# Performance work log

Measured on AMD Instinct MI355X. Metric: run time of the kernel, lower is better.

The kernel has to match this reference:

```python
import jax, jax.numpy as jnp
import numpy as np

B, C, D, H, W = 1, 32, 32, 128, 128


def setup_inputs() -> dict:
    key = jax.random.key(0)
    kx, kq, kk, kv, ko = jax.random.split(key, 5)
    s = 1.0 / np.sqrt(C)
    return {
        "x": jax.random.normal(kx, (B, C, D, H, W), dtype=jnp.float32),
        "Wq": jax.random.normal(kq, (C, C), dtype=jnp.float32) * s,
        "Wk": jax.random.normal(kk, (C, C), dtype=jnp.float32) * s,
        "Wv": jax.random.normal(kv, (C, C), dtype=jnp.float32) * s,
        "Wo": jax.random.normal(ko, (C, C), dtype=jnp.float32) * s,
    }


def reference(x, Wq, Wk, Wv, Wo):
    # x: [B, C, D, H, W]; multi-dimensional (axial) self-attention:
    # independent softmax-attention along each spatial axis, outputs summed.
    scale = jnp.asarray(x.shape[1], x.dtype) ** -0.5
    q = jnp.einsum("bcdhw,oc->bodhw", x, Wq)
    k = jnp.einsum("bcdhw,oc->bodhw", x, Wk)
    v = jnp.einsum("bcdhw,oc->bodhw", x, Wv)

    # attention along D axis: scores [B, H, W, D, D]
    ad = jax.nn.softmax(jnp.einsum("bcdhw,bcehw->bhwde", q, k) * scale, axis=-1)
    od = jnp.einsum("bhwde,bcehw->bcdhw", ad, v)

    # attention along H axis: scores [B, D, W, H, H]
    ah = jax.nn.softmax(jnp.einsum("bcdhw,bcdgw->bdwhg", q, k) * scale, axis=-1)
    oh = jnp.einsum("bdwhg,bcdgw->bcdhw", ah, v)

    # attention along W axis: scores [B, D, H, W, W]
    aw = jax.nn.softmax(jnp.einsum("bcdhw,bcdhu->bdhwu", q, k) * scale, axis=-1)
    ow = jnp.einsum("bdhwu,bcdhu->bcdhw", aw, v)

    out = jnp.einsum("bcdhw,oc->bodhw", od + oh + ow, Wo) + x  # residual
    return out
```

## Files before the change

### kernel.cpp

```cpp
#include <hip/hip_runtime.h>


#define C_ 32
#define D_ 32
#define H_ 128
#define W_ 128
#define SC (D_*H_*W_)
#define SD (H_*W_)
#define SH (W_)
#define SCALE 0.17677669529663687f

typedef __attribute__((ext_vector_type(8))) short short8;
typedef __attribute__((ext_vector_type(4))) short short4v;
typedef __attribute__((ext_vector_type(2))) short short2v;
typedef __attribute__((ext_vector_type(4))) float f32x4;

#define MFMA16(a,b,c) __builtin_amdgcn_mfma_f32_16x16x32_bf16(a,b,c,0,0,0)

__device__ __forceinline__ int xcd_swz(int bid, int nwg) {
    int chunk = nwg >> 3;
    return (bid & 7) * chunk + (bid >> 3);
}
__device__ __forceinline__ short bf16_trunc(float f) {
    return (short)(__float_as_uint(f) >> 16);
}
__device__ __forceinline__ short bf16_rtne(float f) {
    unsigned u = __float_as_uint(f);
    unsigned r = u + 0x7FFFu + ((u >> 16) & 1u);
    return (short)(r >> 16);
}
__device__ __forceinline__ float bf16_tof(short s) {
    return __uint_as_float(((unsigned)(unsigned short)s) << 16);
}
__device__ __forceinline__ short8 ld8_b64x2(const short* p) {
    short4v a = *(const short4v*)p;
    short4v b = *(const short4v*)(p + 4);
    short8 o;
    o[0]=a[0]; o[1]=a[1]; o[2]=a[2]; o[3]=a[3];
    o[4]=b[0]; o[5]=b[1]; o[6]=b[2]; o[7]=b[3];
    return o;
}

__device__ __forceinline__ void compute_Mbf(const float* __restrict__ Wq,
                                            const float* __restrict__ Wk,
                                            short* Mh, short* Ml) {
    for (int o = threadIdx.x; o < 1024; o += 256) {
        int a = o >> 5, b = o & 31;
        float acc = 0.f;
        #pragma unroll
        for (int m = 0; m < 32; ++m) acc += Wq[m*32+a] * Wk[m*32+b];
        acc *= SCALE;
        short h = bf16_trunc(acc);
        Mh[o] = h;
        Ml[o] = bf16_trunc(acc - bf16_tof(h));
    }
}
__device__ __forceinline__ void compute_Pbf(const float* __restrict__ Wv,
                                            const float* __restrict__ Wo,
                                            short* Ph, short* Pl) {
    for (int o = threadIdx.x; o < 1024; o += 256) {
        int oo = o >> 5, c = o & 31;
        float acc = 0.f;
        #pragma unroll
        for (int m = 0; m < 32; ++m) acc += Wo[oo*32+m] * Wv[m*32+c];
        short h = bf16_trunc(acc);
        Ph[o] = h;
        Pl[o] = bf16_trunc(acc - bf16_tof(h));
    }
}

#define TT_STRIDE 40
#define XH_STRIDE 136
#define P_STRIDE  136
#define R_BYTES   36864

__device__ __forceinline__ void slice_engine(
        const float* Xf, const short* Mh, const short* Ml,
        short* Tt_h, short* Tt_l, short* P, short* Xh,
        f32x4 uacc[2][2])
{
    const int t = threadIdx.x;
    const int wv = t >> 6, l = t & 63, hi = l >> 4, r = l & 15;
    const int qb = wv * 32;

    #pragma unroll
    for (int k = 0; k < 8; ++k) {
        int idx = t + k*256;
        int u2 = idx & 63, c = idx >> 6;
        float2 v = *(const float2*)&Xf[c*128 + u2*2];
        short2v h; h[0] = bf16_rtne(v.x); h[1] = bf16_rtne(v.y);
        *(short2v*)&Xh[c*XH_STRIDE + u2*2] = h;
    }

    short8 xh_[2], xl_[2];
    #pragma unroll
    for (int nt = 0; nt < 2; ++nt) {
        int u = qb + nt*16 + r;
        #pragma unroll
        for (int j = 0; j < 8; ++j) {
            float f = Xf[(hi*8 + j)*128 + u];
            short h = bf16_trunc(f);
            xh_[nt][j] = h; xl_[nt][j] = bf16_trunc(f - bf16_tof(h));
        }
    }

    short8 mah[2], mal[2];
    #pragma unroll
    for (int mt = 0; mt < 2; ++mt) {
        mah[mt] = *(const short8*)&Mh[(r + 16*mt)*32 + hi*8];
        mal[mt] = *(const short8*)&Ml[(r + 16*mt)*32 + hi*8];
    }
    f32x4 tacc[2][2] = {};
    #pragma unroll
    for (int nt = 0; nt < 2; ++nt) {
        #pragma unroll
        for (int mt = 0; mt < 2; ++mt) {
            tacc[mt][nt] = MFMA16(mah[mt], xh_[nt], tacc[mt][nt]);
            tacc[mt][nt] = MFMA16(mah[mt], xl_[nt], tacc[mt][nt]);
            tacc[mt][nt] = MFMA16(mal[mt], xh_[nt], tacc[mt][nt]);
        }
    }
    #pragma unroll
    for (int mt = 0; mt < 2; ++mt)
    #pragma unroll
    for (int nt = 0; nt < 2; ++nt) {
        int u = qb + nt*16 + r;
        #pragma unroll
        for (int rp = 0; rp < 2; ++rp) {
            int c0 = 16*mt + 4*hi + 2*rp;
            float f0 = tacc[mt][nt][2*rp], f1 = tacc[mt][nt][2*rp+1];
            short h0 = bf16_trunc(f0), h1 = bf16_trunc(f1);
            short2v vh; vh[0] = h0; vh[1] = h1;
            *(short2v*)&Tt_h[u*TT_STRIDE + c0] = vh;
            short2v vl; vl[0] = bf16_trunc(f0 - bf16_tof(h0));
            vl[1] = bf16_trunc(f1 - bf16_tof(h1));
            *(short2v*)&Tt_l[u*TT_STRIDE + c0] = vl;
        }
    }
    __syncthreads();

    f32x4 sacc[2][8] = {};
    #pragma unroll
    for (int nt = 0; nt < 8; ++nt) {
        short8 th = *(const short8*)&Tt_h[(nt*16 + r)*TT_STRIDE + hi*8];
        short8 tl = *(const short8*)&Tt_l[(nt*16 + r)*TT_STRIDE + hi*8];
        #pragma unroll
        for (int qt = 0; qt < 2; ++qt) {
            sacc[qt][nt] = MFMA16(xh_[qt], th, sacc[qt][nt]);
            sacc[qt][nt] = MFMA16(xh_[qt], tl, sacc[qt][nt]);
            sacc[qt][nt] = MFMA16(xl_[qt], th, sacc[qt][nt]);
        }
    }
    float rls[2][4];
    #pragma unroll
    for (int qt = 0; qt < 2; ++qt)
    #pragma unroll
    for (int reg = 0; reg < 4; ++reg) {
        float m = sacc[qt][0][reg];
        #pragma unroll
        for (int nt = 1; nt < 8; ++nt) m = fmaxf(m, sacc[qt][nt][reg]);
        m = fmaxf(m, __shfl_xor(m, 1));
        m = fmaxf(m, __shfl_xor(m, 2));
        m = fmaxf(m, __shfl_xor(m, 4));
        m = fmaxf(m, __shfl_xor(m, 8));
        float s = 0.f;
        #pragma unroll
        for (int nt = 0; nt < 8; ++nt) {
            float e = __expf(sacc[qt][nt][reg] - m);
            sacc[qt][nt][reg] = e; s += e;
        }
        s += __shfl_xor(s, 1);
        s += __shfl_xor(s, 2);
        s += __shfl_xor(s, 4);
        s += __shfl_xor(s, 8);
        rls[qt][reg] = 1.f / s;
    }
    __syncthreads();
    #pragma unroll
    for (int qt = 0; qt < 2; ++qt)
    #pragma unroll
    for (int reg = 0; reg < 4; ++reg) {
        int q = qb + 16*qt + 4*hi + reg;
        float rl = rls[qt][reg];
        #pragma unroll
        for (int nt = 0; nt < 8; ++nt)
            P[q*P_STRIDE + nt*16 + r] = bf16_rtne(sacc[qt][nt][reg] * rl);
    }
    __syncthreads();

    #pragma unroll
    for (int kt = 0; kt < 4; ++kt) {
        short8 xa[2], pb[2];
        #pragma unroll
        for (int mt = 0; mt < 2; ++mt)
            xa[mt] = *(const short8*)&Xh[(r + 16*mt)*XH_STRIDE + hi*8 + kt*32];
        #pragma unroll
        for (int nt = 0; nt < 2; ++nt)
            pb[nt] = *(const short8*)&P[(qb + 16*nt + r)*P_STRIDE + hi*8 + kt*32];
        #pragma unroll
        for (int mt = 0; mt < 2; ++mt)
        #pragma unroll
        for (int nt = 0; nt < 2; ++nt)
            uacc[mt][nt] = MFMA16(xa[mt], pb[nt], uacc[mt][nt]);
    }
}

__global__ __launch_bounds__(256) void kw_kernel(const float* __restrict__ x,
        const float* __restrict__ Wq, const float* __restrict__ Wk,
        float* __restrict__ U) {
    __shared__ __align__(16) char Rr[R_BYTES];
    __shared__ __align__(16) short Xh[32*XH_STRIDE];
    __shared__ __align__(16) short MhS[1024], MlS[1024];
    float* Xf = (float*)Rr;
    short* Tt_h = (short*)(Rr + 16384);
    short* Tt_l = (short*)(Rr + 26624);
    short* P = (short*)Rr;
    int bid = xcd_swz(blockIdx.x, gridDim.x);
    int d = bid >> 7, h = bid & 127;
    int t = threadIdx.x;
    compute_Mbf(Wq, Wk, MhS, MlS);
    const float* xs = x + d*SD + h*SH;
    #pragma unroll
    for (int k = 0; k < 4; ++k) {
        int idx = t + k*256;
        int c = idx >> 5, u4 = idx & 31;
        *(float4*)&Xf[c*128 + u4*4] = *(const float4*)&xs[c*SC + u4*4];
    }
    __syncthreads();
    f32x4 uacc[2][2] = {};
    slice_engine(Xf, MhS, MlS, Tt_h, Tt_l, P, Xh, uacc);
    const int wv = t >> 6, l = t & 63, hi = l >> 4, r = l & 15;
    float* Uo = U + d*SD + h*SH;
    #pragma unroll
    for (int mt = 0; mt < 2; ++mt)
    #pragma unroll
    for (int nt = 0; nt < 2; ++nt)
    #pragma unroll
    for (int reg = 0; reg < 4; ++reg) {
        int c = 16*mt + 4*hi + reg;
        int q = wv*32 + 16*nt + r;
        Uo[c*SC + q] = uacc[mt][nt][reg];
    }
}

__global__ __launch_bounds__(256) void kh_kernel(const float* __restrict__ x,
        const float* __restrict__ Wq, const float* __restrict__ Wk,
        float* __restrict__ U) {
    __shared__ __align__(16) char Rr[R_BYTES];
    __shared__ __align__(16) float Xf1[32*128];
    __shared__ __align__(16) short Xh[32*XH_STRIDE];
    __shared__ __align__(16) short MhS[1024], MlS[1024];
    float* Xf0 = (float*)Rr;
    short* Tt_h = (short*)(Rr + 16384);
    short* Tt_l = (short*)(Rr + 26624);
    short* P = (short*)Rr;
    int bid = xcd_swz(blockIdx.x, gridDim.x);
    int d = bid >> 6, w0 = (bid & 63) * 2;
    int t = threadIdx.x;
    compute_Mbf(Wq, Wk, MhS, MlS);
    const float* xs = x + d*SD + w0;
    #pragma unroll
    for (int k = 0; k < 16; ++k) {
        int idx = t + k*256;
        int c = idx >> 7, g = idx & 127;
        float2 v = *(const float2*)&xs[c*SC + g*SH];
        Xf0[c*128+g] = v.x;
        Xf1[c*128+g] = v.y;
    }
    __syncthreads();
    f32x4 u0[2][2] = {}, u1[2][2] = {};
    slice_engine(Xf0, MhS, MlS, Tt_h, Tt_l, P, Xh, u0);
    __syncthreads();
    slice_engine(Xf1, MhS, MlS, Tt_h, Tt_l, P, Xh, u1);
    const int wv = t >> 6, l = t & 63, hi = l >> 4, r = l & 15;
    float* Uo = U + d*SD + w0;
    #pragma unroll
    for (int mt = 0; mt < 2; ++mt)
    #pragma unroll
    for (int nt = 0; nt < 2; ++nt)
    #pragma unroll
    for (int reg = 0; reg < 4; ++reg) {
        int c = 16*mt + 4*hi + reg;
        int q = wv*32 + 16*nt + r;
        float2* p = (float2*)&Uo[c*SC + q*SH];
        float2 v = *p;
        v.x += u0[mt][nt][reg];
        v.y += u1[mt][nt][reg];
        *p = v;
    }
}

#define XJ 1152
#define KD_TTS 40
#define KD_PS  36
__global__ __launch_bounds__(256, 2) void kd_kernel(const float* __restrict__ x,
        const float* __restrict__ Wq, const float* __restrict__ Wk,
        const float* __restrict__ Wv, const float* __restrict__ Wo,
        float* __restrict__ UO) {
    __shared__ __align__(16) short Mh[1024], Ml[1024], Psh[1024], Psl[1024];
    __shared__ __align__(16) short Xh[8*XJ], Xl[8*XJ];
    __shared__ __align__(16) char Rr[33792];
    short* Tt_h = (short*)Rr;
    short* Tt_l = (short*)(Rr + 10240);
    short* Pp   = (short*)(Rr + 20480);
    float* u_lds = (float*)Rr;

    int bid = xcd_swz(blockIdx.x, gridDim.x);
    int h = bid >> 4, w0 = (bid & 15) * 8;
    int t = threadIdx.x;
    const int wv = t >> 6, l = t & 63, hi = l >> 4, r = l & 15;

    compute_Mbf(Wq, Wk, Mh, Ml);
    compute_Pbf(Wv, Wo, Psh, Psl);

    const float* xs = x + h*SH + w0;
    #pragma unroll
    for (int k = 0; k < 8; ++k) {
        int o = t + k*256;
        int j4 = o & 1, d = (o >> 1) & 31, c = o >> 6;
        float4 v = *(const float4*)(xs + c*SC + d*SD + j4*4);
        float fr[4] = {v.x, v.y, v.z, v.w};
        #pragma unroll
        for (int i = 0; i < 4; ++i) {
            short hh = bf16_trunc(fr[i]);
            Xh[((j4*4+i)*32 + c)*KD_PS + d] = hh;
            Xl[((j4*4+i)*32 + c)*KD_PS + d] = bf16_trunc(fr[i] - bf16_tof(hh));
        }
    }
    __syncthreads();

    short8 mah[2], mal[2], pah[2], pal[2];
    #pragma unroll
    for (int mt = 0; mt < 2; ++mt) {
        mah[mt] = *(const short8*)&Mh[(mt*16 + r)*32 + hi*8];
        mal[mt] = *(const short8*)&Ml[(mt*16 + r)*32 + hi*8];
        pah[mt] = *(const short8*)&Psh[(mt*16 + r)*32 + hi*8];
        pal[mt] = *(const short8*)&Psl[(mt*16 + r)*32 + hi*8];
    }

    f32x4 uacc[2][2][2] = {};
    float4 upre[8];

    #pragma unroll
    for (int ps = 0; ps < 2; ++ps) {
        int j = ps*4 + wv;
        const short* Xhj = &Xh[j*XJ];
        const short* Xlj = &Xl[j*XJ];
        short8 xph[2], xpl[2];
        #pragma unroll
        for (int et = 0; et < 2; ++et)
        #pragma unroll
        for (int jj = 0; jj < 8; ++jj) {
            int c = hi*8 + jj;
            xph[et][jj] = Xhj[c*KD_PS + et*16 + r];
            xpl[et][jj] = Xlj[c*KD_PS + et*16 + r];
        }
        f32x4 tacc[2][2] = {};
        #pragma unroll
        for (int et = 0; et < 2; ++et)
        #pragma unroll
        for (int mt = 0; mt < 2; ++mt) {
            tacc[mt][et] = MFMA16(mah[mt], xph[et], tacc[mt][et]);
            tacc[mt][et] = MFMA16(mah[mt], xpl[et], tacc[mt][et]);
            tacc[mt][et] = MFMA16(mal[mt], xph[et], tacc[mt][et]);
        }
        int tb = wv*32*KD_TTS;
        #pragma unroll
        for (int mt = 0; mt < 2; ++mt)
        #pragma unroll
        for (int et = 0; et < 2; ++et) {
            int e = et*16 + r;
            #pragma unroll
            for (int rp = 0; rp < 2; ++rp) {
                int c0 = mt*16 + hi*4 + rp*2;
                float f0 = tacc[mt][et][rp*2], f1 = tacc[mt][et][rp*2+1];
                short h0 = bf16_trunc(f0), h1 = bf16_trunc(f1);
                short2v vh; vh[0] = h0; vh[1] = h1;
                *(short2v*)&Tt_h[tb + e*KD_TTS + c0] = vh;
                short2v vl; vl[0] = bf16_trunc(f0 - bf16_tof(h0));
                vl[1] = bf16_trunc(f1 - bf16_tof(h1));
                *(short2v*)&Tt_l[tb + e*KD_TTS + c0] = vl;
            }
        }
        f32x4 sacc[2][2] = {};
        #pragma unroll
        for (int et = 0; et < 2; ++et) {
            short8 th = *(const short8*)&Tt_h[tb + (et*16 + r)*KD_TTS + hi*8];
            short8 tl = *(const short8*)&Tt_l[tb + (et*16 + r)*KD_TTS + hi*8];
            #pragma unroll
            for (int qt = 0; qt < 2; ++qt) {
                sacc[qt][et] = MFMA16(xph[qt], th, sacc[qt][et]);
                sacc[qt][et] = MFMA16(xph[qt], tl, sacc[qt][et]);
                sacc[qt][et] = MFMA16(xpl[qt], th, sacc[qt][et]);
            }
        }
        int pb = wv*32*KD_PS;
        #pragma unroll
        for (int qt = 0; qt < 2; ++qt)
        #pragma unroll
        for (int reg = 0; reg < 4; ++reg) {
            float m = fmaxf(sacc[qt][0][reg], sacc[qt][1][reg]);
            m = fmaxf(m, __shfl_xor(m, 1));
            m = fmaxf(m, __shfl_xor(m, 2));
            m = fmaxf(m, __shfl_xor(m, 4));
            m = fmaxf(m, __shfl_xor(m, 8));
            float e0 = __expf(sacc[qt][0][reg] - m);
            float e1 = __expf(sacc[qt][1][reg] - m);
            float s = e0 + e1;
            s += __shfl_xor(s, 1);
            s += __shfl_xor(s, 2);
            s += __shfl_xor(s, 4);
            s += __shfl_xor(s, 8);
            float rl = 1.f / s;
            int d = qt*16 + hi*4 + reg;
            Pp[pb + d*KD_PS + 0*16 + r] = bf16_rtne(e0 * rl);
            Pp[pb + d*KD_PS + 1*16 + r] = bf16_rtne(e1 * rl);
        }
        #pragma unroll
        for (int mt = 0; mt < 2; ++mt) {
            short8 xa = ld8_b64x2(&Xhj[(mt*16 + r)*KD_PS + hi*8]);
            #pragma unroll
            for (int nt = 0; nt < 2; ++nt) {
                short8 pbf = ld8_b64x2(&Pp[pb + (nt*16 + r)*KD_PS + hi*8]);
                uacc[ps][mt][nt] = MFMA16(xa, pbf, uacc[ps][mt][nt]);
            }
        }
        if (ps == 0) {
            #pragma unroll
            for (int k = 0; k < 8; ++k) {
                int o = t + k*256;
                int j4 = o & 1, d = (o >> 1) & 31, c = o >> 6;
                upre[k] = *(const float4*)(UO + c*SC + d*SD + h*SH + w0 + j4*4);
            }
        }
    }
    __syncthreads();
    #pragma unroll
    for (int k = 0; k < 8; ++k) {
        int o = t + k*256;
        int j4 = o & 1, d = (o >> 1) & 31, c = o >> 6;
        *(float4*)&u_lds[c*264 + d*8 + j4*4] = upre[k];
    }
    __syncthreads();
    #pragma unroll
    for (int ps = 0; ps < 2; ++ps)
    #pragma unroll
    for (int mt = 0; mt < 2; ++mt)
    #pragma unroll
    for (int nt = 0; nt < 2; ++nt)
    #pragma unroll
    for (int reg = 0; reg < 4; ++reg) {
        int c = mt*16 + hi*4 + reg;
        u_lds[c*264 + (nt*16 + r)*8 + ps*4 + wv] += uacc[ps][mt][nt][reg];
    }
    __syncthreads();
    f32x4 eacc[2][4] = {};
    #pragma unroll
    for (int nt = 0; nt < 4; ++nt) {
        short8 bh, bl;
        #pragma unroll
        for (int jj = 0; jj < 8; ++jj) {
            float f = u_lds[(hi*8 + jj)*264 + wv*64 + nt*16 + r];
            short hh = bf16_trunc(f);
            bh[jj] = hh; bl[jj] = bf16_trunc(f - bf16_tof(hh));
        }
        #pragma unroll
        for (int mt = 0; mt < 2; ++mt) {
            eacc[mt][nt] = MFMA16(pah[mt], bh, eacc[mt][nt]);
            eacc[mt][nt] = MFMA16(pah[mt], bl, eacc[mt][nt]);
            eacc[mt][nt] = MFMA16(pal[mt], bh, eacc[mt][nt]);
        }
    }
    #pragma unroll
    for (int mt = 0; mt < 2; ++mt)
    #pragma unroll
    for (int nt = 0; nt < 4; ++nt)
    #pragma unroll
    for (int reg = 0; reg < 4; ++reg) {
        int o = mt*16 + hi*4 + reg;
        int s = wv*64 + nt*16 + r;
        int addr = o*SC + (s >> 3)*SD + h*SH + w0 + (s & 7);
        UO[addr] = eacc[mt][nt][reg] + x[addr];
    }
}

extern "C" void kernel_launch(void* const* d_in, const int* in_sizes, int n_in,
                              void* d_out, int out_size, void* d_ws, size_t ws_size,
                              hipStream_t stream) {
    (void)in_sizes; (void)n_in; (void)out_size; (void)d_ws; (void)ws_size;
    const float* x  = (const float*)d_in[0];
    const float* Wq = (const float*)d_in[1];
    const float* Wk = (const float*)d_in[2];
    const float* Wv = (const float*)d_in[3];
    const float* Wo = (const float*)d_in[4];
    float* U = (float*)d_out;
    kw_kernel<<<dim3(4096), dim3(256), 0, stream>>>(x, Wq, Wk, U);
    kh_kernel<<<dim3(2048), dim3(256), 0, stream>>>(x, Wq, Wk, U);
    kd_kernel<<<dim3(2048), dim3(256), 0, stream>>>(x, Wq, Wk, Wv, Wo, U);
}
```

Baseline: 379.5 us.

## Precompute folded weight matrices once in a small init kernel

Adds a tiny kernel that computes the scaled Wq^T·Wk and Wo·Wv products, split into bf16 hi/lo pairs, once into workspace. Every block of the three attention kernels previously redid this 32x32x32 product, and it now loads its MFMA fragments straight from global memory. The bf16 conversion of X moves into the global load loop. The H-axis kernel changes from two columns per block to one, which drops a shared buffer and doubles the grid, at the cost of losing the float2 read-modify-write pairing. One extra launch is added.

```diff
diff --git a/kernel.cpp b/kernel.cpp
--- a/kernel.cpp
+++ b/kernel.cpp
@@ -41,32 +41,25 @@
     return o;
 }
 
-__device__ __forceinline__ void compute_Mbf(const float* __restrict__ Wq,
-                                            const float* __restrict__ Wk,
-                                            short* Mh, short* Ml) {
-    for (int o = threadIdx.x; o < 1024; o += 256) {
-        int a = o >> 5, b = o & 31;
-        float acc = 0.f;
-        #pragma unroll
-        for (int m = 0; m < 32; ++m) acc += Wq[m*32+a] * Wk[m*32+b];
-        acc *= SCALE;
-        short h = bf16_trunc(acc);
-        Mh[o] = h;
-        Ml[o] = bf16_trunc(acc - bf16_tof(h));
-    }
-}
-__device__ __forceinline__ void compute_Pbf(const float* __restrict__ Wv,
-                                            const float* __restrict__ Wo,
-                                            short* Ph, short* Pl) {
-    for (int o = threadIdx.x; o < 1024; o += 256) {
-        int oo = o >> 5, c = o & 31;
-        float acc = 0.f;
-        #pragma unroll
-        for (int m = 0; m < 32; ++m) acc += Wo[oo*32+m] * Wv[m*32+c];
-        short h = bf16_trunc(acc);
-        Ph[o] = h;
-        Pl[o] = bf16_trunc(acc - bf16_tof(h));
-    }
+__global__ __launch_bounds__(256) void kinit_kernel(
+        const float* __restrict__ Wq, const float* __restrict__ Wk,
+        const float* __restrict__ Wv, const float* __restrict__ Wo,
+        short* __restrict__ ws) {
+    int o = blockIdx.x * 256 + threadIdx.x;
+    int a = o >> 5, b = o & 31;
+    float m = 0.f, p = 0.f;
+    #pragma unroll
+    for (int k = 0; k < 32; ++k) {
+        m += Wq[k*32+a] * Wk[k*32+b];
+        p += Wo[a*32+k] * Wv[k*32+b];
+    }
+    m *= SCALE;
+    short mh = bf16_trunc(m);
+    ws[o]        = mh;
+    ws[1024 + o] = bf16_trunc(m - bf16_tof(mh));
+    short ph = bf16_trunc(p);
+    ws[2048 + o] = ph;
+    ws[3072 + o] = bf16_trunc(p - bf16_tof(ph));
 }
 
 #define TT_STRIDE 40
@@ -75,7 +68,7 @@
 #define R_BYTES   36864
 
 __device__ __forceinline__ void slice_engine(
-        const float* Xf, const short* Mh, const short* Ml,
+        const float* Xf, const short8 mah[2], const short8 mal[2],
         short* Tt_h, short* Tt_l, short* P, short* Xh,
         f32x4 uacc[2][2])
 {
@@ -83,15 +76,6 @@
     const int wv = t >> 6, l = t & 63, hi = l >> 4, r = l & 15;
     const int qb = wv * 32;
 
-    #pragma unroll
-    for (int k = 0; k < 8; ++k) {
-        int idx = t + k*256;
-        int u2 = idx & 63, c = idx >> 6;
-        float2 v = *(const float2*)&Xf[c*128 + u2*2];
-        short2v h; h[0] = bf16_rtne(v.x); h[1] = bf16_rtne(v.y);
-        *(short2v*)&Xh[c*XH_STRIDE + u2*2] = h;
-    }
-
     short8 xh_[2], xl_[2];
     #pragma unroll
     for (int nt = 0; nt < 2; ++nt) {
@@ -104,12 +88,6 @@
         }
     }
 
-    short8 mah[2], mal[2];
-    #pragma unroll
-    for (int mt = 0; mt < 2; ++mt) {
-        mah[mt] = *(const short8*)&Mh[(r + 16*mt)*32 + hi*8];
-        mal[mt] = *(const short8*)&Ml[(r + 16*mt)*32 + hi*8];
-    }
     f32x4 tacc[2][2] = {};
     #pragma unroll
     for (int nt = 0; nt < 2; ++nt) {
@@ -206,11 +184,9 @@
 }
 
 __global__ __launch_bounds__(256) void kw_kernel(const float* __restrict__ x,
-        const float* __restrict__ Wq, const float* __restrict__ Wk,
-        float* __restrict__ U) {
+        const short* __restrict__ ws, float* __restrict__ U) {
     __shared__ __align__(16) char Rr[R_BYTES];
     __shared__ __align__(16) short Xh[32*XH_STRIDE];
-    __shared__ __align__(16) short MhS[1024], MlS[1024];
     float* Xf = (float*)Rr;
     short* Tt_h = (short*)(Rr + 16384);
     short* Tt_l = (short*)(Rr + 26624);
@@ -218,18 +194,28 @@
     int bid = xcd_swz(blockIdx.x, gridDim.x);
     int d = bid >> 7, h = bid & 127;
     int t = threadIdx.x;
-    compute_Mbf(Wq, Wk, MhS, MlS);
+    const int wv = t >> 6, l = t & 63, hi = l >> 4, r = l & 15;
+    short8 mah[2], mal[2];
+    #pragma unroll
+    for (int mt = 0; mt < 2; ++mt) {
+        mah[mt] = *(const short8*)&ws[(r + 16*mt)*32 + hi*8];
+        mal[mt] = *(const short8*)&ws[1024 + (r + 16*mt)*32 + hi*8];
+    }
     const float* xs = x + d*SD + h*SH;
     #pragma unroll
     for (int k = 0; k < 4; ++k) {
         int idx = t + k*256;
         int c = idx >> 5, u4 = idx & 31;
-        *(float4*)&Xf[c*128 + u4*4] = *(const float4*)&xs[c*SC + u4*4];
+        float4 v = *(const float4*)&xs[c*SC + u4*4];
+        *(float4*)&Xf[c*128 + u4*4] = v;
+        short4v hv;
+        hv[0] = bf16_rtne(v.x); hv[1] = bf16_rtne(v.y);
+        hv[2] = bf16_rtne(v.z); hv[3] = bf16_rtne(v.w);
+        *(short4v*)&Xh[c*XH_STRIDE + u4*4] = hv;
     }
     __syncthreads();
     f32x4 uacc[2][2] = {};
-    slice_engine(Xf, MhS, MlS, Tt_h, Tt_l, P, Xh, uacc);
-    const int wv = t >> 6, l = t & 63, hi = l >> 4, r = l & 15;
+    slice_engine(Xf, mah, mal, Tt_h, Tt_l, P, Xh, uacc);
     float* Uo = U + d*SD + h*SH;
     #pragma unroll
     for (int mt = 0; mt < 2; ++mt)
@@ -244,36 +230,36 @@
 }
 
 __global__ __launch_bounds__(256) void kh_kernel(const float* __restrict__ x,
-        const float* __restrict__ Wq, const float* __restrict__ Wk,
-        float* __restrict__ U) {
+        const short* __restrict__ ws, float* __restrict__ U) {
     __shared__ __align__(16) char Rr[R_BYTES];
-    __shared__ __align__(16) float Xf1[32*128];
     __shared__ __align__(16) short Xh[32*XH_STRIDE];
-    __shared__ __align__(16) short MhS[1024], MlS[1024];
-    float* Xf0 = (float*)Rr;
+    float* Xf = (float*)Rr;
     short* Tt_h = (short*)(Rr + 16384);
     short* Tt_l = (short*)(Rr + 26624);
     short* P = (short*)Rr;
     int bid = xcd_swz(blockIdx.x, gridDim.x);
-    int d = bid >> 6, w0 = (bid & 63) * 2;
+    int d = bid >> 7, w = bid & 127;
     int t = threadIdx.x;
-    compute_Mbf(Wq, Wk, MhS, MlS);
-    const float* xs = x + d*SD + w0;
+    const int wv = t >> 6, l = t & 63, hi = l >> 4, r = l & 15;
+    short8 mah[2], mal[2];
+    #pragma unroll
+    for (int mt = 0; mt < 2; ++mt) {
+        mah[mt] = *(const short8*)&ws[(r + 16*mt)*32 + hi*8];
+        mal[mt] = *(const short8*)&ws[1024 + (r + 16*mt)*32 + hi*8];
+    }
+    const float* xs = x + d*SD + w;
     #pragma unroll
     for (int k = 0; k < 16; ++k) {
         int idx = t + k*256;
         int c = idx >> 7, g = idx & 127;
-        float2 v = *(const float2*)&xs[c*SC + g*SH];
-        Xf0[c*128+g] = v.x;
-        Xf1[c*128+g] = v.y;
-    }
-    __syncthreads();
-    f32x4 u0[2][2] = {}, u1[2][2] = {};
-    slice_engine(Xf0, MhS, MlS, Tt_h, Tt_l, P, Xh, u0);
-    __syncthreads();
-    slice_engine(Xf1, MhS, MlS, Tt_h, Tt_l, P, Xh, u1);
-    const int wv = t >> 6, l = t & 63, hi = l >> 4, r = l & 15;
-    float* Uo = U + d*SD + w0;
+        float f = xs[c*SC + g*SH];
+        Xf[c*128 + g] = f;
+        Xh[c*XH_STRIDE + g] = bf16_rtne(f);
+    }
+    __syncthreads();
+    f32x4 uacc[2][2] = {};
+    slice_engine(Xf, mah, mal, Tt_h, Tt_l, P, Xh, uacc);
+    float* Uo = U + d*SD + w;
     #pragma unroll
     for (int mt = 0; mt < 2; ++mt)
     #pragma unroll
@@ -282,11 +268,7 @@
     for (int reg = 0; reg < 4; ++reg) {
         int c = 16*mt + 4*hi + reg;
         int q = wv*32 + 16*nt + r;
-        float2* p = (float2*)&Uo[c*SC + q*SH];
-        float2 v = *p;
-        v.x += u0[mt][nt][reg];
-        v.y += u1[mt][nt][reg];
-        *p = v;
+        Uo[c*SC + q*SH] += uacc[mt][nt][reg];
     }
 }
 
@@ -294,10 +276,7 @@
 #define KD_TTS 40
 #define KD_PS  36
 __global__ __launch_bounds__(256, 2) void kd_kernel(const float* __restrict__ x,
-        const float* __restrict__ Wq, const float* __restrict__ Wk,
-        const float* __restrict__ Wv, const float* __restrict__ Wo,
-        float* __restrict__ UO) {
-    __shared__ __align__(16) short Mh[1024], Ml[1024], Psh[1024], Psl[1024];
+        const short* __restrict__ ws, float* __restrict__ UO) {
     __shared__ __align__(16) short Xh[8*XJ], Xl[8*XJ];
     __shared__ __align__(16) char Rr[33792];
     short* Tt_h = (short*)Rr;
@@ -310,8 +289,14 @@
     int t = threadIdx.x;
     const int wv = t >> 6, l = t & 63, hi = l >> 4, r = l & 15;
 
-    compute_Mbf(Wq, Wk, Mh, Ml);
-    compute_Pbf(Wv, Wo, Psh, Psl);
+    short8 mah[2], mal[2], pah[2], pal[2];
+    #pragma unroll
+    for (int mt = 0; mt < 2; ++mt) {
+        mah[mt] = *(const short8*)&ws[(mt*16 + r)*32 + hi*8];
+        mal[mt] = *(const short8*)&ws[1024 + (mt*16 + r)*32 + hi*8];
+        pah[mt] = *(const short8*)&ws[2048 + (mt*16 + r)*32 + hi*8];
+        pal[mt] = *(const short8*)&ws[3072 + (mt*16 + r)*32 + hi*8];
+    }
 
     const float* xs = x + h*SH + w0;
     #pragma unroll
@@ -328,15 +313,6 @@
         }
     }
     __syncthreads();
-
-    short8 mah[2], mal[2], pah[2], pal[2];
-    #pragma unroll
-    for (int mt = 0; mt < 2; ++mt) {
-        mah[mt] = *(const short8*)&Mh[(mt*16 + r)*32 + hi*8];
-        mal[mt] = *(const short8*)&Ml[(mt*16 + r)*32 + hi*8];
-        pah[mt] = *(const short8*)&Psh[(mt*16 + r)*32 + hi*8];
-        pal[mt] = *(const short8*)&Psl[(mt*16 + r)*32 + hi*8];
-    }
 
     f32x4 uacc[2][2][2] = {};
     float4 upre[8];
@@ -487,14 +463,16 @@
 extern "C" void kernel_launch(void* const* d_in, const int* in_sizes, int n_in,
                               void* d_out, int out_size, void* d_ws, size_t ws_size,
                               hipStream_t stream) {
-    (void)in_sizes; (void)n_in; (void)out_size; (void)d_ws; (void)ws_size;
+    (void)in_sizes; (void)n_in; (void)out_size; (void)ws_size;
     const float* x  = (const float*)d_in[0];
     const float* Wq = (const float*)d_in[1];
     const float* Wk = (const float*)d_in[2];
     const float* Wv = (const float*)d_in[3];
     const float* Wo = (const float*)d_in[4];
+    short* ws = (short*)d_ws;
     float* U = (float*)d_out;
-    kw_kernel<<<dim3(4096), dim3(256), 0, stream>>>(x, Wq, Wk, U);
-    kh_kernel<<<dim3(2048), dim3(256), 0, stream>>>(x, Wq, Wk, U);
-    kd_kernel<<<dim3(2048), dim3(256), 0, stream>>>(x, Wq, Wk, Wv, Wo, U);
-}
+    kinit_kernel<<<dim3(4), dim3(256), 0, stream>>>(Wq, Wk, Wv, Wo, ws);
+    kw_kernel<<<dim3(4096), dim3(256), 0, stream>>>(x, ws, U);
+    kh_kernel<<<dim3(4096), dim3(256), 0, stream>>>(x, ws, U);
+    kd_kernel<<<dim3(2048), dim3(256), 0, stream>>>(x, ws, U);
+}
```

Result: slower. 430.7 us (+13.5%).
